# Optimization experiments

Hardware: AMD Instinct MI355X
Metric: run time of the kernel (lower is better)

The kernel has to match this reference:

```python
import jax, jax.numpy as jnp
import numpy as np

B, C_IN, C_OUT, N = 4096, 256, 256, 25


def setup_inputs() -> dict:
    key = jax.random.key(0)
    k_x, k_adj, k_w, k_b = jax.random.split(key, 4)
    x = jax.random.normal(k_x, (B, C_IN, N), dtype=jnp.float32)
    adj = jax.random.uniform(k_adj, (N, N), dtype=jnp.float32)
    # Conv1d(C_in, C_out, 1) weight is [C_out, C_in, 1]; drop trailing 1.
    W = jax.random.normal(k_w, (C_OUT, C_IN), dtype=jnp.float32) * (1.0 / np.sqrt(C_IN))
    b = jax.random.normal(k_b, (C_OUT,), dtype=jnp.float32) * 0.01
    return {"x": x, "adj": adj, "W": W, "b": b}


def reference(x, adj, W, b):
    # 1x1 Conv1d == per-node linear transform: [B, C_out, N]
    support = jnp.einsum('oc,bcn->bon', W, x) + b[None, :, None]
    # Dense adjacency aggregation: support @ adj.T -> [B, C_out, N]
    output = jnp.einsum('bon,mn->bom', support, adj)
    # dropout=0 (disabled); in_features == out_features -> identity residual
    return jax.nn.relu(output + x)
```

## Files before the change

### kernel.cpp

```cpp
#include <hip/hip_runtime.h>
#include <hip/hip_bf16.h>


#define BATCH 4096
#define C 256
#define N 25
#define NB 8
#define XSTR 28
#define YSTR 264

typedef __bf16 bf16x8 __attribute__((ext_vector_type(8)));
typedef float f32x4 __attribute__((ext_vector_type(4)));

__global__ void prep_kernel(const float* __restrict__ W, const float* __restrict__ adj,
                            bf16x8* __restrict__ Wshuf, float* __restrict__ adjS) {
    int i = blockIdx.x * 256 + threadIdx.x;
    int f = i >> 6, l = i & 63;
    int T = f >> 3, kk = f & 7;
    int quad = l >> 4, l15 = l & 15;
    int o = T * 16 + l15;
    int cb = kk * 32 + quad * 8;
    bf16x8 v;
    #pragma unroll
    for (int j = 0; j < 8; ++j) v[j] = (__bf16)W[o * C + cb + j];
    Wshuf[i] = v;
    if (blockIdx.x == 0 && threadIdx.x < 32) {
        float s = 0.f;
        if (threadIdx.x < N)
            for (int n = 0; n < N; ++n) s += adj[threadIdx.x * N + n];
        adjS[threadIdx.x] = s;
    }
}

__global__ __launch_bounds__(512, 4) void gcn_kernel(
    const float* __restrict__ x, const float* __restrict__ adj,
    const float* __restrict__ bias, const float* __restrict__ adjSg,
    const bf16x8* __restrict__ Wshuf, float* __restrict__ out)
{
    __shared__ __align__(16) float  xs[C * XSTR];
    __shared__ __align__(16) __bf16 ys[32 * YSTR];
    __shared__ __align__(16) float  outS[C * N];
    __shared__ __align__(16) __bf16 adjbf[32 * 40];
    __shared__ float biasS[C];

    const int tid = threadIdx.x;
    const int wv = tid >> 6, lane = tid & 63;
    const int quad = lane >> 4, l15 = lane & 15;
    const int o0 = wv * 32;
    const int b0 = blockIdx.x * NB;

    for (int e = tid; e < N * N; e += 512) {
        int m = e / N, n = e - m * N;
        adjbf[m * 40 + n] = (__bf16)adj[e];
    }
    if (tid < N) {
        #pragma unroll
        for (int n = N; n < 32; ++n) adjbf[tid * 40 + n] = (__bf16)0.f;
    } else if (tid < 32) {
        #pragma unroll
        for (int n = 0; n < 32; ++n) adjbf[tid * 40 + n] = (__bf16)0.f;
    }
    if (tid < C) biasS[tid] = bias[tid];

    bf16x8 af[8][2];
    #pragma unroll
    for (int kk = 0; kk < 8; ++kk)
        #pragma unroll
        for (int ot = 0; ot < 2; ++ot)
            af[kk][ot] = Wshuf[(((wv * 2 + ot) * 8 + kk) << 6) + lane];

    const float aS0 = adjSg[l15];
    const float aS1 = adjSg[16 + l15];

    __syncthreads();

    const bf16x8 a0 = *(const bf16x8*)&adjbf[l15 * 40 + quad * 8];
    const bf16x8 a1 = *(const bf16x8*)&adjbf[(16 + l15) * 40 + quad * 8];

    {
        const float* xb = x + (size_t)b0 * (C * N);
        float4 r0[4];
        #pragma unroll
        for (int rr = 0; rr < 4; ++rr)
            if (rr < 3 || lane < 8) r0[rr] = ((const float4*)xb)[wv * 200 + rr * 64 + lane];
        #pragma unroll
        for (int rr = 0; rr < 4; ++rr)
            if (rr < 3 || lane < 8) {
                int e = (wv * 200 + rr * 64 + lane) * 4;
                int c = e / N, n = e - c * N;
                float fv[4] = {r0[rr].x, r0[rr].y, r0[rr].z, r0[rr].w};
                #pragma unroll
                for (int j = 0; j < 4; ++j) {
                    xs[c * XSTR + n] = fv[j];
                    ++n; if (n == N) { n = 0; ++c; }
                }
            }
    }

    #pragma unroll 1
    for (int bi = 0; bi < NB; ++bi) {
        float* outb = out + (size_t)(b0 + bi) * (C * N);

        float4 rn[4];
        const bool pf = (bi + 1 < NB);
        if (pf) {
            const float* xb = x + (size_t)(b0 + bi + 1) * (C * N);
            #pragma unroll
            for (int rr = 0; rr < 4; ++rr)
                if (rr < 3 || lane < 8) rn[rr] = ((const float4*)xb)[wv * 200 + rr * 64 + lane];
        }

        #pragma unroll
        for (int ctl = 0; ctl < 2; ++ctl) {
            const int c = o0 + ctl * 16 + l15;
            bf16x8 xf;
            if (quad < 3) {
                f32x4 u = *(const f32x4*)&xs[c * XSTR + quad * 8];
                f32x4 w = *(const f32x4*)&xs[c * XSTR + quad * 8 + 4];
                xf[0]=(__bf16)u[0]; xf[1]=(__bf16)u[1]; xf[2]=(__bf16)u[2]; xf[3]=(__bf16)u[3];
                xf[4]=(__bf16)w[0]; xf[5]=(__bf16)w[1]; xf[6]=(__bf16)w[2]; xf[7]=(__bf16)w[3];
            } else {
                float u = xs[c * XSTR + 24];
                xf[0] = (__bf16)u;
                #pragma unroll
                for (int j = 1; j < 8; ++j) xf[j] = (__bf16)0.f;
            }
            f32x4 y0 = __builtin_amdgcn_mfma_f32_16x16x32_bf16(a0, xf, (f32x4)0.f, 0, 0, 0);
            f32x4 y1 = __builtin_amdgcn_mfma_f32_16x16x32_bf16(a1, xf, (f32x4)0.f, 0, 0, 0);
            #pragma unroll
            for (int r2 = 0; r2 < 4; ++r2) {
                ys[(quad * 4 + r2) * YSTR + c]      = (__bf16)y0[r2];
                ys[(16 + quad * 4 + r2) * YSTR + c] = (__bf16)y1[r2];
            }
        }
        asm volatile("s_waitcnt lgkmcnt(0)\n\ts_barrier" ::: "memory");

        f32x4 acc[2][2];
        #pragma unroll
        for (int ot = 0; ot < 2; ++ot) { acc[ot][0] = (f32x4)0.f; acc[ot][1] = (f32x4)0.f; }
        #pragma unroll
        for (int kk = 0; kk < 8; ++kk) {
            bf16x8 bfr0 = *(const bf16x8*)&ys[l15 * YSTR + kk * 32 + quad * 8];
            bf16x8 bfr1 = *(const bf16x8*)&ys[(16 + l15) * YSTR + kk * 32 + quad * 8];
            #pragma unroll
            for (int ot = 0; ot < 2; ++ot) {
                acc[ot][0] = __builtin_amdgcn_mfma_f32_16x16x32_bf16(af[kk][ot], bfr0, acc[ot][0], 0, 0, 0);
                acc[ot][1] = __builtin_amdgcn_mfma_f32_16x16x32_bf16(af[kk][ot], bfr1, acc[ot][1], 0, 0, 0);
            }
        }

        #pragma unroll
        for (int ot = 0; ot < 2; ++ot)
            #pragma unroll
            for (int r2 = 0; r2 < 4; ++r2) {
                const int o = o0 + ot * 16 + quad * 4 + r2;
                const float bia = biasS[o];
                {
                    const int m = l15;
                    float v = acc[ot][0][r2] + bia * aS0 + xs[o * XSTR + m];
                    outS[o * N + m] = v > 0.f ? v : 0.f;
                }
                if (l15 < N - 16) {
                    const int m = 16 + l15;
                    float v = acc[ot][1][r2] + bia * aS1 + xs[o * XSTR + m];
                    outS[o * N + m] = v > 0.f ? v : 0.f;
                }
            }

        if (pf) {
            #pragma unroll
            for (int rr = 0; rr < 4; ++rr)
                if (rr < 3 || lane < 8) {
                    int e = (wv * 200 + rr * 64 + lane) * 4;
                    int c = e / N, n = e - c * N;
                    float fv[4] = {rn[rr].x, rn[rr].y, rn[rr].z, rn[rr].w};
                    #pragma unroll
                    for (int j = 0; j < 4; ++j) {
                        xs[c * XSTR + n] = fv[j];
                        ++n; if (n == N) { n = 0; ++c; }
                    }
                }
        }

        #pragma unroll
        for (int rr = 0; rr < 4; ++rr)
            if (rr < 3 || lane < 8) {
                int i4 = wv * 200 + rr * 64 + lane;
                ((float4*)outb)[i4] = ((const float4*)outS)[i4];
            }

        asm volatile("s_barrier" ::: "memory");
    }
}

extern "C" void kernel_launch(void* const* d_in, const int* in_sizes, int n_in,
                              void* d_out, int out_size, void* d_ws, size_t ws_size,
                              hipStream_t stream) {
    (void)in_sizes; (void)n_in; (void)out_size; (void)ws_size;
    const float* x    = (const float*)d_in[0];
    const float* adj  = (const float*)d_in[1];
    const float* W    = (const float*)d_in[2];
    const float* bias = (const float*)d_in[3];
    float* out = (float*)d_out;

    unsigned char* ws = (unsigned char*)d_ws;
    bf16x8* Wshuf = (bf16x8*)ws;
    float*  adjS  = (float*)(ws + 131072);

    prep_kernel<<<32, 256, 0, stream>>>(W, adj, Wshuf, adjS);
    gcn_kernel<<<BATCH / NB, 512, 0, stream>>>(x, adj, bias, adjS, Wshuf, out);
}
```

Baseline: 248.6 us.

## Double-buffer x tiles in LDS via direct global-to-LDS async loads

Replaces the register-staged prefetch and per-element scatter into a padded xs buffer with global_load_lds transfers straight into a double-buffered, unpadded LDS tile. Explicit vmcnt waits let each iteration's next-batch load stay in flight while the current batch is computed. The ys staging buffer is aliased onto outS, with an extra barrier to protect it, to fit the second x buffer. This removes the VALU and LDS-write cost of the scatter but drops the XSTR padding, which may add LDS bank conflicts. It also depends on hand-counted vmcnt values that include the output stores.

```diff
diff --git a/kernel.cpp b/kernel.cpp
--- a/kernel.cpp
+++ b/kernel.cpp
@@ -6,11 +6,16 @@
 #define C 256
 #define N 25
 #define NB 8
-#define XSTR 28
+#define XW 6400
 #define YSTR 264
 
 typedef __bf16 bf16x8 __attribute__((ext_vector_type(8)));
 typedef float f32x4 __attribute__((ext_vector_type(4)));
+
+#define GLOAD16(gp, lp)                                                        \
+    __builtin_amdgcn_global_load_lds(                                          \
+        (const __attribute__((address_space(1))) unsigned int*)(gp),           \
+        (__attribute__((address_space(3))) unsigned int*)(lp), 16, 0, 0)
 
 __global__ void prep_kernel(const float* __restrict__ W, const float* __restrict__ adj,
                             bf16x8* __restrict__ Wshuf, float* __restrict__ adjS) {
@@ -37,11 +42,11 @@
     const float* __restrict__ bias, const float* __restrict__ adjSg,
     const bf16x8* __restrict__ Wshuf, float* __restrict__ out)
 {
-    __shared__ __align__(16) float  xs[C * XSTR];
-    __shared__ __align__(16) __bf16 ys[32 * YSTR];
-    __shared__ __align__(16) float  outS[C * N];
+    __shared__ __align__(16) float  xs2[2][XW];
+    __shared__ __align__(16) float  outS[XW];
     __shared__ __align__(16) __bf16 adjbf[32 * 40];
     __shared__ float biasS[C];
+    __bf16* const ys = (__bf16*)outS;
 
     const int tid = threadIdx.x;
     const int wv = tid >> 6, lane = tid & 63;
@@ -78,50 +83,44 @@
     const bf16x8 a1 = *(const bf16x8*)&adjbf[(16 + l15) * 40 + quad * 8];
 
     {
-        const float* xb = x + (size_t)b0 * (C * N);
-        float4 r0[4];
+        const float4* xb = (const float4*)(x + (size_t)b0 * XW);
         #pragma unroll
         for (int rr = 0; rr < 4; ++rr)
-            if (rr < 3 || lane < 8) r0[rr] = ((const float4*)xb)[wv * 200 + rr * 64 + lane];
-        #pragma unroll
-        for (int rr = 0; rr < 4; ++rr)
-            if (rr < 3 || lane < 8) {
-                int e = (wv * 200 + rr * 64 + lane) * 4;
-                int c = e / N, n = e - c * N;
-                float fv[4] = {r0[rr].x, r0[rr].y, r0[rr].z, r0[rr].w};
-                #pragma unroll
-                for (int j = 0; j < 4; ++j) {
-                    xs[c * XSTR + n] = fv[j];
-                    ++n; if (n == N) { n = 0; ++c; }
-                }
-            }
+            if (rr < 3 || lane < 8)
+                GLOAD16(xb + (wv * 200 + rr * 64 + lane),
+                        &xs2[0][(wv * 200 + rr * 64) * 4]);
     }
 
     #pragma unroll 1
     for (int bi = 0; bi < NB; ++bi) {
-        float* outb = out + (size_t)(b0 + bi) * (C * N);
+        const int cur = bi & 1;
+        float* outb = out + (size_t)(b0 + bi) * XW;
+        const bool pf = (bi + 1 < NB);
 
-        float4 rn[4];
-        const bool pf = (bi + 1 < NB);
         if (pf) {
-            const float* xb = x + (size_t)(b0 + bi + 1) * (C * N);
+            const float4* xb = (const float4*)(x + (size_t)(b0 + bi + 1) * XW);
             #pragma unroll
             for (int rr = 0; rr < 4; ++rr)
-                if (rr < 3 || lane < 8) rn[rr] = ((const float4*)xb)[wv * 200 + rr * 64 + lane];
+                if (rr < 3 || lane < 8)
+                    GLOAD16(xb + (wv * 200 + rr * 64 + lane),
+                            &xs2[cur ^ 1][(wv * 200 + rr * 64) * 4]);
         }
+
+        if (bi == 0 || !pf) asm volatile("s_waitcnt vmcnt(4)" ::: "memory");
+        else                asm volatile("s_waitcnt vmcnt(8)" ::: "memory");
+
+        const float* xc = xs2[cur];
 
         #pragma unroll
         for (int ctl = 0; ctl < 2; ++ctl) {
             const int c = o0 + ctl * 16 + l15;
+            const float* xr = xc + c * N;
             bf16x8 xf;
             if (quad < 3) {
-                f32x4 u = *(const f32x4*)&xs[c * XSTR + quad * 8];
-                f32x4 w = *(const f32x4*)&xs[c * XSTR + quad * 8 + 4];
-                xf[0]=(__bf16)u[0]; xf[1]=(__bf16)u[1]; xf[2]=(__bf16)u[2]; xf[3]=(__bf16)u[3];
-                xf[4]=(__bf16)w[0]; xf[5]=(__bf16)w[1]; xf[6]=(__bf16)w[2]; xf[7]=(__bf16)w[3];
+                #pragma unroll
+                for (int j = 0; j < 8; ++j) xf[j] = (__bf16)xr[quad * 8 + j];
             } else {
-                float u = xs[c * XSTR + 24];
-                xf[0] = (__bf16)u;
+                xf[0] = (__bf16)xr[24];
                 #pragma unroll
                 for (int j = 1; j < 8; ++j) xf[j] = (__bf16)0.f;
             }
@@ -148,6 +147,7 @@
                 acc[ot][1] = __builtin_amdgcn_mfma_f32_16x16x32_bf16(af[kk][ot], bfr1, acc[ot][1], 0, 0, 0);
             }
         }
+        asm volatile("s_barrier" ::: "memory");
 
         #pragma unroll
         for (int ot = 0; ot < 2; ++ot)
@@ -157,30 +157,15 @@
                 const float bia = biasS[o];
                 {
                     const int m = l15;
-                    float v = acc[ot][0][r2] + bia * aS0 + xs[o * XSTR + m];
+                    float v = acc[ot][0][r2] + bia * aS0 + xc[o * N + m];
                     outS[o * N + m] = v > 0.f ? v : 0.f;
                 }
                 if (l15 < N - 16) {
                     const int m = 16 + l15;
-                    float v = acc[ot][1][r2] + bia * aS1 + xs[o * XSTR + m];
+                    float v = acc[ot][1][r2] + bia * aS1 + xc[o * N + m];
                     outS[o * N + m] = v > 0.f ? v : 0.f;
                 }
             }
-
-        if (pf) {
-            #pragma unroll
-            for (int rr = 0; rr < 4; ++rr)
-                if (rr < 3 || lane < 8) {
-                    int e = (wv * 200 + rr * 64 + lane) * 4;
-                    int c = e / N, n = e - c * N;
-                    float fv[4] = {rn[rr].x, rn[rr].y, rn[rr].z, rn[rr].w};
-                    #pragma unroll
-                    for (int j = 0; j < 4; ++j) {
-                        xs[c * XSTR + n] = fv[j];
-                        ++n; if (n == N) { n = 0; ++c; }
-                    }
-                }
-        }
 
         #pragma unroll
         for (int rr = 0; rr < 4; ++rr)
```

Result: faster. 204.5 us (-17.7%).
